# Performance work log

Hardware: AMD Instinct MI355X
Metric: run time of the kernel (lower is better)

Reference implementation:

```python
import jax, jax.numpy as jnp
import numpy as np

WINDOW = 127          # odd
W = (WINDOW - 1) // 2 # 63 half-window
Q_CH = WINDOW + 1     # 128 query chunk
K_CH = WINDOW * 2     # 254 key chunk


def _compl_mod(m, n):
    return int(n * int(np.ceil(m / n)) - m)


def setup_inputs() -> dict:
    key = jax.random.key(0)
    kq, kk, kv = jax.random.split(key, 3)
    B, L, NH, H = 4, 4096, 16, 64
    return {
        "q": jax.random.normal(kq, (B, L, NH, H), dtype=jnp.float32),
        "k": jax.random.normal(kk, (B, L, NH, H), dtype=jnp.float32),
        "v": jax.random.normal(kv, (B, L, NH, H), dtype=jnp.float32),
    }


def _build_mask(c, k_pad, dtype_bool=bool):
    # base band mask over one (q_ch, k_ch) block: True = masked out
    u = jnp.triu(jnp.ones((Q_CH, K_CH), dtype=bool))
    band = jnp.logical_and(u, jnp.flip(u, (0, 1)))
    base = ~band
    mask_left = base.at[:, :W].set(True)
    mask_right = base.at[:, K_CH - (W + k_pad):].set(True)
    if c > 1:
        mid = jnp.broadcast_to(base, (c - 2, Q_CH, K_CH)) if c > 2 else jnp.zeros((0, Q_CH, K_CH), bool)
        return jnp.concatenate([mask_left[None], mid, mask_right[None]], axis=0)
    return jnp.logical_or(mask_left, mask_right)[None]


def reference(q, k, v):
    b, s, nh, h = q.shape
    q = q * (h ** -0.5)

    q_pad = _compl_mod(s, Q_CH)
    k_pad = _compl_mod(s + 2 * W - K_CH, Q_CH)

    # chunk queries: (b, c, q_ch, nh, h)
    qp = jnp.pad(q, ((0, 0), (0, q_pad), (0, 0), (0, 0)))
    c = (s + q_pad) // Q_CH
    qw = qp.reshape(b, c, Q_CH, nh, h)

    # overlapping key/value windows via gather: (b, c, k_ch, nh, h)
    kp = jnp.pad(k, ((0, 0), (W, W + k_pad), (0, 0), (0, 0)))
    vp = jnp.pad(v, ((0, 0), (W, W + k_pad), (0, 0), (0, 0)))
    starts = np.arange(c) * Q_CH
    idx = starts[:, None] + np.arange(K_CH)[None, :]  # (c, k_ch)
    kw = kp[:, idx]
    vw = vp[:, idx]

    # block scores: (b, nh, c, q_ch, k_ch)
    A = jnp.einsum('bcqnh,bcknh->bncqk', qw, kw)

    mask = _build_mask(c, k_pad)  # (c, q_ch, k_ch)
    neg = -jnp.finfo(A.dtype).max
    A = jnp.where(mask[None, None], neg, A)
    A = jax.nn.softmax(A, axis=-1)

    z = jnp.einsum('bncqk,bcknh->bncqh', A, vw)  # (b, nh, c, q_ch, h)
    z = z.reshape(b, nh, c * Q_CH, h)[:, :, :s]
    return jnp.transpose(z, (0, 2, 1, 3))  # (b, s, nh, h)
```

## Files before the change

### kernel.cpp

```cpp
#include <hip/hip_runtime.h>


typedef _Float16 f16;
typedef _Float16 f16x2  __attribute__((ext_vector_type(2)));
typedef _Float16 f16x4  __attribute__((ext_vector_type(4)));
typedef _Float16 f16x8  __attribute__((ext_vector_type(8)));
typedef float    f32x16 __attribute__((ext_vector_type(16)));
typedef int      int4v  __attribute__((ext_vector_type(4)));

constexpr int NB = 4, L = 4096, NH = 16, H = 64;
constexpr int CQ = 128, NC = L / CQ, KW = 256, WR = 63;
constexpr int RS = NH * H;

constexpr int Q_OFF = 0;
constexpr int K_OFF = 16384;
constexpr int V_OFF = 49152;
constexpr int LDS_BYTES = 81920;

#define DEV static __device__ __forceinline__

DEV int iclamp(int x, int lo, int hi) { return x < lo ? lo : (x > hi ? hi : x); }

DEV float fexp2(float x) {
#if __has_builtin(__builtin_amdgcn_exp2f)
    return __builtin_amdgcn_exp2f(x);
#else
    return exp2f(x);
#endif
}

DEV int packh2(float a, float b) {
    f16x2 p; p.x = (f16)a; p.y = (f16)b;
    return __builtin_bit_cast(int, p);
}

DEV int rmaddr(int base, int r, int colb) {
    return base + r * 128 + (colb ^ ((r & 7) << 4));
}

DEV int vaddr(int h, int kb) {
    return V_OFF + ((h * 512 + kb) ^ ((((h & 7) ^ ((h >> 3) & 7))) << 4));
}

DEV void swap_halves(int& a, int& b) {
    asm volatile("v_permlane32_swap_b32 %0, %1" : "+v"(a), "+v"(b));
}

__global__ __launch_bounds__(512, 4)
void wattn_kernel(const float* __restrict__ q_, const float* __restrict__ k_,
                  const float* __restrict__ v_, float* __restrict__ o_)
{
    __shared__ alignas(16) char smem[LDS_BYTES];
    float* O_lds = (float*)smem;
    float* D_lds = (float*)(smem + 32768);

    const int bid = (int)blockIdx.x;
    const int wid = (bid & 7) * ((NB * NH * NC) / 8) + (bid >> 3);
    const int c = wid & (NC - 1);
    const int n = (wid >> 5) & (NH - 1);
    const int b = wid >> 9;

    const int t    = (int)threadIdx.x;
    const int lane = t & 63;
    const int w    = t >> 6;
    const int lq   = lane & 31;
    const int hi   = lane >> 5;
    const int qt   = w & 3;
    const int half = w >> 2;

    const int kg0 = c * CQ - WR;
    const size_t bn = ((size_t)b * L * NH + n) * H;
    const float qs = 0.125f * 1.44269504088896f;

    const int h4 = (t & 15) << 2;
    const int cb = h4 << 1;
    const int ru = t >> 4;

    {
        const float* qp = q_ + bn + (size_t)(c * CQ) * RS + h4;
        #pragma unroll
        for (int p = 0; p < 4; ++p) {
            int r = ru + p * 32;
            float4 x = *(const float4*)(qp + (size_t)r * RS);
            *(f16x4*)(smem + rmaddr(Q_OFF, r, cb)) =
                (f16x4){(f16)(x.x * qs), (f16)(x.y * qs), (f16)(x.z * qs), (f16)(x.w * qs)};
        }
    }
    #pragma unroll
    for (int p = 0; p < 8; ++p) {
        int r  = ru + p * 32;
        int kr = iclamp(kg0 + r, 0, L - 1);
        float4 x = *(const float4*)(k_ + bn + (size_t)kr * RS + h4);
        *(f16x4*)(smem + rmaddr(K_OFF, r, cb)) =
            (f16x4){(f16)x.x, (f16)x.y, (f16)x.z, (f16)x.w};
    }
    #pragma unroll
    for (int p = 0; p < 4; ++p) {
        int r0  = ru * 2 + p * 64;
        int kr0 = iclamp(kg0 + r0,     0, L - 1);
        int kr1 = iclamp(kg0 + r0 + 1, 0, L - 1);
        float4 v0 = *(const float4*)(v_ + bn + (size_t)kr0 * RS + h4);
        float4 v1 = *(const float4*)(v_ + bn + (size_t)kr1 * RS + h4);
        int kb = r0 * 2;
        *(f16x2*)(smem + vaddr(h4 + 0, kb)) = (f16x2){(f16)v0.x, (f16)v1.x};
        *(f16x2*)(smem + vaddr(h4 + 1, kb)) = (f16x2){(f16)v0.y, (f16)v1.y};
        *(f16x2*)(smem + vaddr(h4 + 2, kb)) = (f16x2){(f16)v0.z, (f16)v1.z};
        *(f16x2*)(smem + vaddr(h4 + 3, kb)) = (f16x2){(f16)v0.w, (f16)v1.w};
    }

    const int iq  = qt * 32 + lq;
    const int jlo = (c == 0) ? WR : 0;
    const int jhi = (KW < L - kg0) ? KW : (L - kg0);
    const int lo  = (iq > jlo) ? iq : jlo;
    const int hb  = (iq + 126 < jhi - 1) ? (iq + 126) : (jhi - 1);
    const unsigned span = (unsigned)(hb - lo);

    f32x16 o0, o1;
    #pragma unroll
    for (int r = 0; r < 16; ++r) { o0[r] = 0.f; o1[r] = 0.f; }
    float dsum = 0.f;

    __syncthreads();

    f16x8 qf[4];
    #pragma unroll
    for (int tq = 0; tq < 4; ++tq)
        qf[tq] = *(const f16x8*)(smem + rmaddr(Q_OFF, qt * 32 + lq, 32 * tq + 16 * hi));

    auto body = [&](int kt) {
        f16x8 kf[4];
        #pragma unroll
        for (int tq = 0; tq < 4; ++tq)
            kf[tq] = *(const f16x8*)(smem + rmaddr(K_OFF, kt * 32 + lq, 32 * tq + 16 * hi));

        f32x16 s;
        #pragma unroll
        for (int r = 0; r < 16; ++r) s[r] = 0.f;
        #pragma unroll
        for (int tq = 0; tq < 4; ++tq)
            s = __builtin_amdgcn_mfma_f32_32x32x16_f16(kf[tq], qf[tq], s, 0, 0, 0);

        const int jb = kt * 32 + 4 * hi;
        float pe[16];
        #pragma unroll
        for (int r = 0; r < 16; ++r) {
            int j = jb + (r & 3) + ((r >> 2) << 3);
            float e = fexp2(s[r]);
            e = ((unsigned)(j - lo) <= span) ? e : 0.f;
            dsum += e;
            pe[r] = e;
        }
        int d0 = packh2(pe[0],  pe[1]),  d1 = packh2(pe[2],  pe[3]);
        int d2 = packh2(pe[4],  pe[5]),  d3 = packh2(pe[6],  pe[7]);
        int d4 = packh2(pe[8],  pe[9]),  d5 = packh2(pe[10], pe[11]);
        int d6 = packh2(pe[12], pe[13]), d7 = packh2(pe[14], pe[15]);
        swap_halves(d0, d2); swap_halves(d1, d3);
        swap_halves(d4, d6); swap_halves(d5, d7);
        f16x8 pa0 = __builtin_bit_cast(f16x8, (int4v){d0, d1, d2, d3});
        f16x8 pa1 = __builtin_bit_cast(f16x8, (int4v){d4, d5, d6, d7});

        const int kb = kt * 64 + hi * 16;
        f16x8 vb00 = *(const f16x8*)(smem + vaddr(lq,      kb));
        f16x8 vb01 = *(const f16x8*)(smem + vaddr(lq,      kb + 32));
        f16x8 vb10 = *(const f16x8*)(smem + vaddr(32 + lq, kb));
        f16x8 vb11 = *(const f16x8*)(smem + vaddr(32 + lq, kb + 32));
        o0 = __builtin_amdgcn_mfma_f32_32x32x16_f16(vb00, pa0, o0, 0, 0, 0);
        o0 = __builtin_amdgcn_mfma_f32_32x32x16_f16(vb01, pa1, o0, 0, 0, 0);
        o1 = __builtin_amdgcn_mfma_f32_32x32x16_f16(vb10, pa0, o1, 0, 0, 0);
        o1 = __builtin_amdgcn_mfma_f32_32x32x16_f16(vb11, pa1, o1, 0, 0, 0);
    };

    const int kt0 = qt + half * 3;
    body(kt0);
    body(kt0 + 1);
    if (!half) body(kt0 + 2);

    float dw = dsum + __shfl_xor(dsum, 32, 64);

    __syncthreads();

    if (!half) {
        #pragma unroll
        for (int r = 0; r < 16; ++r) {
            int h = (r & 3) + ((r >> 2) << 3) + 4 * hi;
            O_lds[h * 128 + iq]        = o0[r];
            O_lds[(32 + h) * 128 + iq] = o1[r];
        }
        if (lane < 32) D_lds[iq] = dw;
    }
    __syncthreads();

    if (half) {
        float dinv = 1.0f / (dw + D_lds[iq]);
        const size_t ob = ((size_t)b * L + (size_t)c * CQ) * RS + (size_t)n * H;
        float* orow = o_ + ob + (size_t)iq * RS;
        #pragma unroll
        for (int m = 0; m < 4; ++m) {
            int h0 = 8 * m + 4 * hi;
            float4 v0, v1;
            v0.x = (o0[4 * m + 0] + O_lds[(h0 + 0) * 128 + iq]) * dinv;
            v0.y = (o0[4 * m + 1] + O_lds[(h0 + 1) * 128 + iq]) * dinv;
            v0.z = (o0[4 * m + 2] + O_lds[(h0 + 2) * 128 + iq]) * dinv;
            v0.w = (o0[4 * m + 3] + O_lds[(h0 + 3) * 128 + iq]) * dinv;
            v1.x = (o1[4 * m + 0] + O_lds[(32 + h0 + 0) * 128 + iq]) * dinv;
            v1.y = (o1[4 * m + 1] + O_lds[(32 + h0 + 1) * 128 + iq]) * dinv;
            v1.z = (o1[4 * m + 2] + O_lds[(32 + h0 + 2) * 128 + iq]) * dinv;
            v1.w = (o1[4 * m + 3] + O_lds[(32 + h0 + 3) * 128 + iq]) * dinv;
            *(float4*)(orow + h0)      = v0;
            *(float4*)(orow + 32 + h0) = v1;
        }
    }
}

extern "C" void kernel_launch(void* const* d_in, const int* in_sizes, int n_in,
                              void* d_out, int out_size, void* d_ws, size_t ws_size,
                              hipStream_t stream) {
    const float* q = (const float*)d_in[0];
    const float* k = (const float*)d_in[1];
    const float* v = (const float*)d_in[2];
    float* o = (float*)d_out;
    (void)in_sizes; (void)n_in; (void)out_size; (void)d_ws; (void)ws_size;
    wattn_kernel<<<dim3(NB * NH * NC), dim3(512), 0, stream>>>(q, k, v, o);
}
```

Measured before the change: 50.51 us.

## Halve block size, load Q to registers, and alias K/V in one LDS buffer

The block shrinks from 512 to 256 threads, so each wave owns one 32-query tile and handles all 5 key tiles itself. This removes the cross-half reduction of partial outputs and denominators through LDS. Q is loaded straight from global memory into registers. K and V share a single 32KB LDS region: the QK scores are computed first and kept as 10 packed f16x8 registers, then V is loaded over the K data behind extra barriers. The intent is less LDS per block and higher occupancy, at the cost of more registers per thread, serialised K-then-V loading, and more global loads per thread.

```diff
diff --git a/kernel.cpp b/kernel.cpp
--- a/kernel.cpp
+++ b/kernel.cpp
@@ -11,11 +11,7 @@
 constexpr int NB = 4, L = 4096, NH = 16, H = 64;
 constexpr int CQ = 128, NC = L / CQ, KW = 256, WR = 63;
 constexpr int RS = NH * H;
-
-constexpr int Q_OFF = 0;
-constexpr int K_OFF = 16384;
-constexpr int V_OFF = 49152;
-constexpr int LDS_BYTES = 81920;
+constexpr int LDS_BYTES = 32768;
 
 #define DEV static __device__ __forceinline__
 
@@ -34,25 +30,23 @@
     return __builtin_bit_cast(int, p);
 }
 
-DEV int rmaddr(int base, int r, int colb) {
-    return base + r * 128 + (colb ^ ((r & 7) << 4));
+DEV int kaddr(int r, int colb) {
+    return r * 128 + (colb ^ ((r & 7) << 4));
 }
 
 DEV int vaddr(int h, int kb) {
-    return V_OFF + ((h * 512 + kb) ^ ((((h & 7) ^ ((h >> 3) & 7))) << 4));
+    return (h * 512 + kb) ^ ((((h & 7) ^ ((h >> 3) & 7))) << 4);
 }
 
 DEV void swap_halves(int& a, int& b) {
     asm volatile("v_permlane32_swap_b32 %0, %1" : "+v"(a), "+v"(b));
 }
 
-__global__ __launch_bounds__(512, 4)
+__global__ __launch_bounds__(256, 4)
 void wattn_kernel(const float* __restrict__ q_, const float* __restrict__ k_,
                   const float* __restrict__ v_, float* __restrict__ o_)
 {
     __shared__ alignas(16) char smem[LDS_BYTES];
-    float* O_lds = (float*)smem;
-    float* D_lds = (float*)(smem + 32768);
 
     const int bid = (int)blockIdx.x;
     const int wid = (bid & 7) * ((NB * NH * NC) / 8) + (bid >> 3);
@@ -65,8 +59,6 @@
     const int w    = t >> 6;
     const int lq   = lane & 31;
     const int hi   = lane >> 5;
-    const int qt   = w & 3;
-    const int half = w >> 2;
 
     const int kg0 = c * CQ - WR;
     const size_t bn = ((size_t)b * L * NH + n) * H;
@@ -76,62 +68,43 @@
     const int cb = h4 << 1;
     const int ru = t >> 4;
 
-    {
-        const float* qp = q_ + bn + (size_t)(c * CQ) * RS + h4;
-        #pragma unroll
-        for (int p = 0; p < 4; ++p) {
-            int r = ru + p * 32;
-            float4 x = *(const float4*)(qp + (size_t)r * RS);
-            *(f16x4*)(smem + rmaddr(Q_OFF, r, cb)) =
-                (f16x4){(f16)(x.x * qs), (f16)(x.y * qs), (f16)(x.z * qs), (f16)(x.w * qs)};
-        }
+    const int iq = w * 32 + lq;
+    const float* qrow = q_ + bn + (size_t)(c * CQ + iq) * RS + hi * 8;
+    f16x8 qf[4];
+    #pragma unroll
+    for (int tq = 0; tq < 4; ++tq) {
+        float4 a  = *(const float4*)(qrow + tq * 16);
+        float4 b2 = *(const float4*)(qrow + tq * 16 + 4);
+        qf[tq] = (f16x8){(f16)(a.x * qs),  (f16)(a.y * qs),  (f16)(a.z * qs),  (f16)(a.w * qs),
+                         (f16)(b2.x * qs), (f16)(b2.y * qs), (f16)(b2.z * qs), (f16)(b2.w * qs)};
     }
+
     #pragma unroll
-    for (int p = 0; p < 8; ++p) {
-        int r  = ru + p * 32;
+    for (int p = 0; p < 16; ++p) {
+        int r  = ru + p * 16;
         int kr = iclamp(kg0 + r, 0, L - 1);
         float4 x = *(const float4*)(k_ + bn + (size_t)kr * RS + h4);
-        *(f16x4*)(smem + rmaddr(K_OFF, r, cb)) =
-            (f16x4){(f16)x.x, (f16)x.y, (f16)x.z, (f16)x.w};
-    }
-    #pragma unroll
-    for (int p = 0; p < 4; ++p) {
-        int r0  = ru * 2 + p * 64;
-        int kr0 = iclamp(kg0 + r0,     0, L - 1);
-        int kr1 = iclamp(kg0 + r0 + 1, 0, L - 1);
-        float4 v0 = *(const float4*)(v_ + bn + (size_t)kr0 * RS + h4);
-        float4 v1 = *(const float4*)(v_ + bn + (size_t)kr1 * RS + h4);
-        int kb = r0 * 2;
-        *(f16x2*)(smem + vaddr(h4 + 0, kb)) = (f16x2){(f16)v0.x, (f16)v1.x};
-        *(f16x2*)(smem + vaddr(h4 + 1, kb)) = (f16x2){(f16)v0.y, (f16)v1.y};
-        *(f16x2*)(smem + vaddr(h4 + 2, kb)) = (f16x2){(f16)v0.z, (f16)v1.z};
-        *(f16x2*)(smem + vaddr(h4 + 3, kb)) = (f16x2){(f16)v0.w, (f16)v1.w};
+        *(f16x4*)(smem + kaddr(r, cb)) = (f16x4){(f16)x.x, (f16)x.y, (f16)x.z, (f16)x.w};
     }
 
-    const int iq  = qt * 32 + lq;
     const int jlo = (c == 0) ? WR : 0;
     const int jhi = (KW < L - kg0) ? KW : (L - kg0);
     const int lo  = (iq > jlo) ? iq : jlo;
     const int hb  = (iq + 126 < jhi - 1) ? (iq + 126) : (jhi - 1);
     const unsigned span = (unsigned)(hb - lo);
 
-    f32x16 o0, o1;
-    #pragma unroll
-    for (int r = 0; r < 16; ++r) { o0[r] = 0.f; o1[r] = 0.f; }
     float dsum = 0.f;
+    f16x8 pa[5][2];
 
     __syncthreads();
 
-    f16x8 qf[4];
     #pragma unroll
-    for (int tq = 0; tq < 4; ++tq)
-        qf[tq] = *(const f16x8*)(smem + rmaddr(Q_OFF, qt * 32 + lq, 32 * tq + 16 * hi));
-
-    auto body = [&](int kt) {
+    for (int i = 0; i < 5; ++i) {
+        const int kt = w + i;
         f16x8 kf[4];
         #pragma unroll
         for (int tq = 0; tq < 4; ++tq)
-            kf[tq] = *(const f16x8*)(smem + rmaddr(K_OFF, kt * 32 + lq, 32 * tq + 16 * hi));
+            kf[tq] = *(const f16x8*)(smem + kaddr(kt * 32 + lq, 32 * tq + 16 * hi));
 
         f32x16 s;
         #pragma unroll
@@ -156,59 +129,60 @@
         int d6 = packh2(pe[12], pe[13]), d7 = packh2(pe[14], pe[15]);
         swap_halves(d0, d2); swap_halves(d1, d3);
         swap_halves(d4, d6); swap_halves(d5, d7);
-        f16x8 pa0 = __builtin_bit_cast(f16x8, (int4v){d0, d1, d2, d3});
-        f16x8 pa1 = __builtin_bit_cast(f16x8, (int4v){d4, d5, d6, d7});
+        pa[i][0] = __builtin_bit_cast(f16x8, (int4v){d0, d1, d2, d3});
+        pa[i][1] = __builtin_bit_cast(f16x8, (int4v){d4, d5, d6, d7});
+    }
 
+    __syncthreads();
+
+    #pragma unroll
+    for (int p = 0; p < 8; ++p) {
+        int r0  = ru * 2 + p * 32;
+        int kr0 = iclamp(kg0 + r0,     0, L - 1);
+        int kr1 = iclamp(kg0 + r0 + 1, 0, L - 1);
+        float4 v0 = *(const float4*)(v_ + bn + (size_t)kr0 * RS + h4);
+        float4 v1 = *(const float4*)(v_ + bn + (size_t)kr1 * RS + h4);
+        int kb = r0 * 2;
+        *(f16x2*)(smem + vaddr(h4 + 0, kb)) = (f16x2){(f16)v0.x, (f16)v1.x};
+        *(f16x2*)(smem + vaddr(h4 + 1, kb)) = (f16x2){(f16)v0.y, (f16)v1.y};
+        *(f16x2*)(smem + vaddr(h4 + 2, kb)) = (f16x2){(f16)v0.z, (f16)v1.z};
+        *(f16x2*)(smem + vaddr(h4 + 3, kb)) = (f16x2){(f16)v0.w, (f16)v1.w};
+    }
+
+    f32x16 o0, o1;
+    #pragma unroll
+    for (int r = 0; r < 16; ++r) { o0[r] = 0.f; o1[r] = 0.f; }
+
+    __syncthreads();
+
+    #pragma unroll
+    for (int i = 0; i < 5; ++i) {
+        const int kt = w + i;
         const int kb = kt * 64 + hi * 16;
         f16x8 vb00 = *(const f16x8*)(smem + vaddr(lq,      kb));
         f16x8 vb01 = *(const f16x8*)(smem + vaddr(lq,      kb + 32));
         f16x8 vb10 = *(const f16x8*)(smem + vaddr(32 + lq, kb));
         f16x8 vb11 = *(const f16x8*)(smem + vaddr(32 + lq, kb + 32));
-        o0 = __builtin_amdgcn_mfma_f32_32x32x16_f16(vb00, pa0, o0, 0, 0, 0);
-        o0 = __builtin_amdgcn_mfma_f32_32x32x16_f16(vb01, pa1, o0, 0, 0, 0);
-        o1 = __builtin_amdgcn_mfma_f32_32x32x16_f16(vb10, pa0, o1, 0, 0, 0);
-        o1 = __builtin_amdgcn_mfma_f32_32x32x16_f16(vb11, pa1, o1, 0, 0, 0);
-    };
+        o0 = __builtin_amdgcn_mfma_f32_32x32x16_f16(vb00, pa[i][0], o0, 0, 0, 0);
+        o0 = __builtin_amdgcn_mfma_f32_32x32x16_f16(vb01, pa[i][1], o0, 0, 0, 0);
+        o1 = __builtin_amdgcn_mfma_f32_32x32x16_f16(vb10, pa[i][0], o1, 0, 0, 0);
+        o1 = __builtin_amdgcn_mfma_f32_32x32x16_f16(vb11, pa[i][1], o1, 0, 0, 0);
+    }
 
-    const int kt0 = qt + half * 3;
-    body(kt0);
-    body(kt0 + 1);
-    if (!half) body(kt0 + 2);
-
-    float dw = dsum + __shfl_xor(dsum, 32, 64);
-
-    __syncthreads();
-
-    if (!half) {
-        #pragma unroll
-        for (int r = 0; r < 16; ++r) {
-            int h = (r & 3) + ((r >> 2) << 3) + 4 * hi;
-            O_lds[h * 128 + iq]        = o0[r];
-            O_lds[(32 + h) * 128 + iq] = o1[r];
-        }
-        if (lane < 32) D_lds[iq] = dw;
-    }
-    __syncthreads();
-
-    if (half) {
-        float dinv = 1.0f / (dw + D_lds[iq]);
-        const size_t ob = ((size_t)b * L + (size_t)c * CQ) * RS + (size_t)n * H;
-        float* orow = o_ + ob + (size_t)iq * RS;
-        #pragma unroll
-        for (int m = 0; m < 4; ++m) {
-            int h0 = 8 * m + 4 * hi;
-            float4 v0, v1;
-            v0.x = (o0[4 * m + 0] + O_lds[(h0 + 0) * 128 + iq]) * dinv;
-            v0.y = (o0[4 * m + 1] + O_lds[(h0 + 1) * 128 + iq]) * dinv;
-            v0.z = (o0[4 * m + 2] + O_lds[(h0 + 2) * 128 + iq]) * dinv;
-            v0.w = (o0[4 * m + 3] + O_lds[(h0 + 3) * 128 + iq]) * dinv;
-            v1.x = (o1[4 * m + 0] + O_lds[(32 + h0 + 0) * 128 + iq]) * dinv;
-            v1.y = (o1[4 * m + 1] + O_lds[(32 + h0 + 1) * 128 + iq]) * dinv;
-            v1.z = (o1[4 * m + 2] + O_lds[(32 + h0 + 2) * 128 + iq]) * dinv;
-            v1.w = (o1[4 * m + 3] + O_lds[(32 + h0 + 3) * 128 + iq]) * dinv;
-            *(float4*)(orow + h0)      = v0;
-            *(float4*)(orow + 32 + h0) = v1;
-        }
+    float dtot = dsum + __shfl_xor(dsum, 32, 64);
+    float dinv = 1.0f / dtot;
+    const size_t ob = ((size_t)b * L + (size_t)c * CQ) * RS + (size_t)n * H;
+    float* orow = o_ + ob + (size_t)iq * RS;
+    #pragma unroll
+    for (int m = 0; m < 4; ++m) {
+        int h0 = 8 * m + 4 * hi;
+        float4 v0, v1;
+        v0.x = o0[4 * m + 0] * dinv;  v0.y = o0[4 * m + 1] * dinv;
+        v0.z = o0[4 * m + 2] * dinv;  v0.w = o0[4 * m + 3] * dinv;
+        v1.x = o1[4 * m + 0] * dinv;  v1.y = o1[4 * m + 1] * dinv;
+        v1.z = o1[4 * m + 2] * dinv;  v1.w = o1[4 * m + 3] * dinv;
+        *(float4*)(orow + h0)      = v0;
+        *(float4*)(orow + 32 + h0) = v1;
     }
 }
 
@@ -220,5 +194,5 @@
     const float* v = (const float*)d_in[2];
     float* o = (float*)d_out;
     (void)in_sizes; (void)n_in; (void)out_size; (void)d_ws; (void)ws_size;
-    wattn_kernel<<<dim3(NB * NH * NC), dim3(512), 0, stream>>>(q, k, v, o);
+    wattn_kernel<<<dim3(NB * NH * NC), dim3(256), 0, stream>>>(q, k, v, o);
 }
```

After: 58.57 us. 16.0% more time.

## Split key tiles across three wave groups with 768-thread blocks

Applied to the files above, without the earlier changes.

Each block now has 12 waves instead of 8, so every query tile's five key tiles are split 2/2/1 across three wave groups rather than 3/2. Two groups write partial outputs and denominators to separate LDS regions, and the first group reduces them and writes the result. The global-to-LDS load is recast as a flat loop over 768 threads. This shortens the per-wave critical path and raises wave count, at the cost of an extra LDS partial buffer, a three-way reduction, and a higher register-pressure launch bound (768, 6).

```diff
diff --git a/kernel.cpp b/kernel.cpp
--- a/kernel.cpp
+++ b/kernel.cpp
@@ -16,6 +16,10 @@
 constexpr int K_OFF = 16384;
 constexpr int V_OFF = 49152;
 constexpr int LDS_BYTES = 81920;
+constexpr int X1_OFF = 0;
+constexpr int X2_OFF = 32768;
+constexpr int D1_OFF = 65536;
+constexpr int D2_OFF = 66048;
 
 #define DEV static __device__ __forceinline__
 
@@ -46,13 +50,11 @@
     asm volatile("v_permlane32_swap_b32 %0, %1" : "+v"(a), "+v"(b));
 }
 
-__global__ __launch_bounds__(512, 4)
+__global__ __launch_bounds__(768, 6)
 void wattn_kernel(const float* __restrict__ q_, const float* __restrict__ k_,
                   const float* __restrict__ v_, float* __restrict__ o_)
 {
     __shared__ alignas(16) char smem[LDS_BYTES];
-    float* O_lds = (float*)smem;
-    float* D_lds = (float*)(smem + 32768);
 
     const int bid = (int)blockIdx.x;
     const int wid = (bid & 7) * ((NB * NH * NC) / 8) + (bid >> 3);
@@ -66,46 +68,43 @@
     const int lq   = lane & 31;
     const int hi   = lane >> 5;
     const int qt   = w & 3;
-    const int half = w >> 2;
+    const int part = w >> 2;
 
     const int kg0 = c * CQ - WR;
     const size_t bn = ((size_t)b * L * NH + n) * H;
     const float qs = 0.125f * 1.44269504088896f;
 
-    const int h4 = (t & 15) << 2;
-    const int cb = h4 << 1;
-    const int ru = t >> 4;
-
-    {
-        const float* qp = q_ + bn + (size_t)(c * CQ) * RS + h4;
-        #pragma unroll
-        for (int p = 0; p < 4; ++p) {
-            int r = ru + p * 32;
-            float4 x = *(const float4*)(qp + (size_t)r * RS);
+    #pragma unroll
+    for (int it = 0; it < 11; ++it) {
+        int flat = it * 768 + t;
+        if (flat < 2048) {
+            int r  = flat >> 4;
+            int cb = (flat & 15) << 3;
+            float4 x = *(const float4*)(q_ + bn + (size_t)(c * CQ + r) * RS + ((flat & 15) << 2));
             *(f16x4*)(smem + rmaddr(Q_OFF, r, cb)) =
                 (f16x4){(f16)(x.x * qs), (f16)(x.y * qs), (f16)(x.z * qs), (f16)(x.w * qs)};
-        }
-    }
-    #pragma unroll
-    for (int p = 0; p < 8; ++p) {
-        int r  = ru + p * 32;
-        int kr = iclamp(kg0 + r, 0, L - 1);
-        float4 x = *(const float4*)(k_ + bn + (size_t)kr * RS + h4);
-        *(f16x4*)(smem + rmaddr(K_OFF, r, cb)) =
-            (f16x4){(f16)x.x, (f16)x.y, (f16)x.z, (f16)x.w};
-    }
-    #pragma unroll
-    for (int p = 0; p < 4; ++p) {
-        int r0  = ru * 2 + p * 64;
-        int kr0 = iclamp(kg0 + r0,     0, L - 1);
-        int kr1 = iclamp(kg0 + r0 + 1, 0, L - 1);
-        float4 v0 = *(const float4*)(v_ + bn + (size_t)kr0 * RS + h4);
-        float4 v1 = *(const float4*)(v_ + bn + (size_t)kr1 * RS + h4);
-        int kb = r0 * 2;
-        *(f16x2*)(smem + vaddr(h4 + 0, kb)) = (f16x2){(f16)v0.x, (f16)v1.x};
-        *(f16x2*)(smem + vaddr(h4 + 1, kb)) = (f16x2){(f16)v0.y, (f16)v1.y};
-        *(f16x2*)(smem + vaddr(h4 + 2, kb)) = (f16x2){(f16)v0.z, (f16)v1.z};
-        *(f16x2*)(smem + vaddr(h4 + 3, kb)) = (f16x2){(f16)v0.w, (f16)v1.w};
+        } else if (flat < 6144) {
+            int j  = flat - 2048;
+            int r  = j >> 4;
+            int cb = (j & 15) << 3;
+            int kr = iclamp(kg0 + r, 0, L - 1);
+            float4 x = *(const float4*)(k_ + bn + (size_t)kr * RS + ((j & 15) << 2));
+            *(f16x4*)(smem + rmaddr(K_OFF, r, cb)) =
+                (f16x4){(f16)x.x, (f16)x.y, (f16)x.z, (f16)x.w};
+        } else if (flat < 8192) {
+            int j   = flat - 6144;
+            int r0  = (j >> 4) << 1;
+            int h4  = (j & 15) << 2;
+            int kr0 = iclamp(kg0 + r0,     0, L - 1);
+            int kr1 = iclamp(kg0 + r0 + 1, 0, L - 1);
+            float4 v0 = *(const float4*)(v_ + bn + (size_t)kr0 * RS + h4);
+            float4 v1 = *(const float4*)(v_ + bn + (size_t)kr1 * RS + h4);
+            int kb = r0 * 2;
+            *(f16x2*)(smem + vaddr(h4 + 0, kb)) = (f16x2){(f16)v0.x, (f16)v1.x};
+            *(f16x2*)(smem + vaddr(h4 + 1, kb)) = (f16x2){(f16)v0.y, (f16)v1.y};
+            *(f16x2*)(smem + vaddr(h4 + 2, kb)) = (f16x2){(f16)v0.z, (f16)v1.z};
+            *(f16x2*)(smem + vaddr(h4 + 3, kb)) = (f16x2){(f16)v0.w, (f16)v1.w};
+        }
     }
 
     const int iq  = qt * 32 + lq;
@@ -170,42 +169,54 @@
         o1 = __builtin_amdgcn_mfma_f32_32x32x16_f16(vb11, pa1, o1, 0, 0, 0);
     };
 
-    const int kt0 = qt + half * 3;
-    body(kt0);
-    body(kt0 + 1);
-    if (!half) body(kt0 + 2);
+    if (part == 0)      { body(qt);     body(qt + 1); }
+    else if (part == 1) { body(qt + 2); body(qt + 3); }
+    else                { body(qt + 4); }
 
     float dw = dsum + __shfl_xor(dsum, 32, 64);
 
     __syncthreads();
 
-    if (!half) {
+    if (part == 1) {
+        float* X = (float*)(smem + X1_OFF);
         #pragma unroll
         for (int r = 0; r < 16; ++r) {
             int h = (r & 3) + ((r >> 2) << 3) + 4 * hi;
-            O_lds[h * 128 + iq]        = o0[r];
-            O_lds[(32 + h) * 128 + iq] = o1[r];
-        }
-        if (lane < 32) D_lds[iq] = dw;
+            X[h * 128 + iq]        = o0[r];
+            X[(32 + h) * 128 + iq] = o1[r];
+        }
+        if (lane < 32) ((float*)(smem + D1_OFF))[iq] = dw;
+    } else if (part == 2) {
+        float* X = (float*)(smem + X2_OFF);
+        #pragma unroll
+        for (int r = 0; r < 16; ++r) {
+            int h = (r & 3) + ((r >> 2) << 3) + 4 * hi;
+            X[h * 128 + iq]        = o0[r];
+            X[(32 + h) * 128 + iq] = o1[r];
+        }
+        if (lane < 32) ((float*)(smem + D2_OFF))[iq] = dw;
     }
     __syncthreads();
 
-    if (half) {
-        float dinv = 1.0f / (dw + D_lds[iq]);
+    if (part == 0) {
+        const float* X1 = (const float*)(smem + X1_OFF);
+        const float* X2 = (const float*)(smem + X2_OFF);
+        float dinv = 1.0f / (dw + ((const float*)(smem + D1_OFF))[iq]
+                                + ((const float*)(smem + D2_OFF))[iq]);
         const size_t ob = ((size_t)b * L + (size_t)c * CQ) * RS + (size_t)n * H;
         float* orow = o_ + ob + (size_t)iq * RS;
         #pragma unroll
         for (int m = 0; m < 4; ++m) {
             int h0 = 8 * m + 4 * hi;
             float4 v0, v1;
-            v0.x = (o0[4 * m + 0] + O_lds[(h0 + 0) * 128 + iq]) * dinv;
-            v0.y = (o0[4 * m + 1] + O_lds[(h0 + 1) * 128 + iq]) * dinv;
-            v0.z = (o0[4 * m + 2] + O_lds[(h0 + 2) * 128 + iq]) * dinv;
-            v0.w = (o0[4 * m + 3] + O_lds[(h0 + 3) * 128 + iq]) * dinv;
-            v1.x = (o1[4 * m + 0] + O_lds[(32 + h0 + 0) * 128 + iq]) * dinv;
-            v1.y = (o1[4 * m + 1] + O_lds[(32 + h0 + 1) * 128 + iq]) * dinv;
-            v1.z = (o1[4 * m + 2] + O_lds[(32 + h0 + 2) * 128 + iq]) * dinv;
-            v1.w = (o1[4 * m + 3] + O_lds[(32 + h0 + 3) * 128 + iq]) * dinv;
+            v0.x = (o0[4 * m + 0] + X1[(h0 + 0) * 128 + iq] + X2[(h0 + 0) * 128 + iq]) * dinv;
+            v0.y = (o0[4 * m + 1] + X1[(h0 + 1) * 128 + iq] + X2[(h0 + 1) * 128 + iq]) * dinv;
+            v0.z = (o0[4 * m + 2] + X1[(h0 + 2) * 128 + iq] + X2[(h0 + 2) * 128 + iq]) * dinv;
+            v0.w = (o0[4 * m + 3] + X1[(h0 + 3) * 128 + iq] + X2[(h0 + 3) * 128 + iq]) * dinv;
+            v1.x = (o1[4 * m + 0] + X1[(32 + h0 + 0) * 128 + iq] + X2[(32 + h0 + 0) * 128 + iq]) * dinv;
+            v1.y = (o1[4 * m + 1] + X1[(32 + h0 + 1) * 128 + iq] + X2[(32 + h0 + 1) * 128 + iq]) * dinv;
+            v1.z = (o1[4 * m + 2] + X1[(32 + h0 + 2) * 128 + iq] + X2[(32 + h0 + 2) * 128 + iq]) * dinv;
+            v1.w = (o1[4 * m + 3] + X1[(32 + h0 + 3) * 128 + iq] + X2[(32 + h0 + 3) * 128 + iq]) * dinv;
             *(float4*)(orow + h0)      = v0;
             *(float4*)(orow + 32 + h0) = v1;
         }
@@ -220,5 +231,5 @@
     const float* v = (const float*)d_in[2];
     float* o = (float*)d_out;
     (void)in_sizes; (void)n_in; (void)out_size; (void)d_ws; (void)ws_size;
-    wattn_kernel<<<dim3(NB * NH * NC), dim3(512), 0, stream>>>(q, k, v, o);
-}
+    wattn_kernel<<<dim3(NB * NH * NC), dim3(768), 0, stream>>>(q, k, v, o);
+}
```

After: 65.41 us. 29.5% more time.
